# Optimization experiments

Measured on AMD Instinct MI355X. Metric: run time of the kernel, lower is better.

Reference implementation:

```python
import jax, jax.numpy as jnp
import numpy as np
from jax import lax

B, P, DIM, HEADS, K = 2, 4096, 256, 8, 32
DH = DIM // HEADS
SCALE = DH ** -0.5


def setup_inputs() -> dict:
    key = jax.random.key(0)
    ks = jax.random.split(key, 12)
    s = 0.02
    return {
        "xyz": jax.random.uniform(ks[0], (B, P, 3), dtype=jnp.float32),
        "feats": jax.random.normal(ks[1], (B, P, DIM), dtype=jnp.float32),
        "Wq": jax.random.normal(ks[2], (DIM, DIM), dtype=jnp.float32) * s,
        "Wk": jax.random.normal(ks[3], (DIM, DIM), dtype=jnp.float32) * s,
        "Wv": jax.random.normal(ks[4], (DIM, DIM), dtype=jnp.float32) * s,
        "Wp": jax.random.normal(ks[5], (DIM, DIM), dtype=jnp.float32) * s,
        "bp": jnp.zeros((DIM,), jnp.float32),
        "W1": jax.random.normal(ks[6], (DIM, 3), dtype=jnp.float32) * s,
        "b1": jnp.zeros((DIM,), jnp.float32),
        "W2": jax.random.normal(ks[7], (DIM, DIM), dtype=jnp.float32) * s,
        "b2": jnp.zeros((DIM,), jnp.float32),
    }


def _gather(points, idx):
    # points: (B,N,C), idx: (B,M,K) -> (B,M,K,C)
    return jax.vmap(lambda p, i: p[i])(points, idx)


def reference(xyz, feats, Wq, Wk, Wv, Wp, bp, W1, b1, W2, b2):
    b, p, d = feats.shape
    # kNN via squared euclidean distance (same ordering as cdist)
    d2 = jnp.sum((xyz[:, :, None, :] - xyz[:, None, :, :]) ** 2, axis=-1)  # (B,P,P)
    _, idx = lax.top_k(-d2, K)  # (B,P,K) smallest distances

    neigh_xyz = _gather(xyz, idx)                      # (B,P,K,3)
    relpos = neigh_xyz - xyz[:, :, None, :]            # (B,P,K,3)

    q = (feats @ Wq.T).reshape(b, p, HEADS, DH)        # (B,P,H,Dh)
    k_full = feats @ Wk.T                              # (B,P,D)
    v_full = feats @ Wv.T
    k_nei = _gather(k_full, idx).reshape(b, p, K, HEADS, DH)
    v_nei = _gather(v_full, idx).reshape(b, p, K, HEADS, DH)

    # pos MLP: Linear(3,dim) -> ReLU -> Linear(dim,dim)
    h = jax.nn.relu(relpos @ W1.T + b1)
    pos_bias = (h @ W2.T + b2).reshape(b, p, K, HEADS, DH)

    attn = jnp.einsum('bphd,bpkhd->bpkh', q, k_nei + pos_bias) * SCALE
    attn = jax.nn.softmax(attn, axis=2)                # over K neighbors
    out = jnp.einsum('bpkh,bpkhd->bphd', attn, v_nei + pos_bias).reshape(b, p, d)
    return out @ Wp.T + bp
```

## Files before the change

kernel.cpp:

```cpp
#include <hip/hip_runtime.h>
#include <cstddef>

#define PB 4096
static constexpr float SCALE_F = 0.17677669529663687f;

typedef __attribute__((ext_vector_type(8))) short bf16x8;
typedef __attribute__((ext_vector_type(4))) float f32x4;

static __device__ __forceinline__ unsigned short f2bf(float x) {
  unsigned u = __builtin_bit_cast(unsigned, x);
  u += 0x7fffu + ((u >> 16) & 1u);
  return (unsigned short)(u >> 16);
}
static __device__ __forceinline__ float bf2f(unsigned short h) {
  return __builtin_bit_cast(float, (unsigned)h << 16);
}

__global__ __launch_bounds__(256) void knn_kernel(const float* __restrict__ xyz,
                                                  int* __restrict__ idx_out) {
  __shared__ float xs[768];
  const int wid = threadIdx.x >> 6;
  const int lane = threadIdx.x & 63;
  const int g = (blockIdx.x << 2) + wid;
  const int b = g >> 12;
  const int p = g & (PB - 1);
  const float* base = xyz + (size_t)b * PB * 3;
  const float qx = base[p * 3 + 0];
  const float qy = base[p * 3 + 1];
  const float qz = base[p * 3 + 2];
  float list_d = 3.4e38f;
  int list_i = -1;
  for (int c = 0; c < 16; ++c) {
    __syncthreads();
    const int src = c * 768 + threadIdx.x;
    xs[threadIdx.x]       = base[src];
    xs[threadIdx.x + 256] = base[src + 256];
    xs[threadIdx.x + 512] = base[src + 512];
    __syncthreads();
#pragma unroll
    for (int s = 0; s < 4; ++s) {
      const int jl = (s << 6) + lane;
      const float dx = __fsub_rn(qx, xs[jl * 3 + 0]);
      const float dy = __fsub_rn(qy, xs[jl * 3 + 1]);
      const float dz = __fsub_rn(qz, xs[jl * 3 + 2]);
      const float d2 = __fadd_rn(__fadd_rn(__fmul_rn(dx, dx), __fmul_rn(dy, dy)),
                                 __fmul_rn(dz, dz));
      float worst = __shfl(list_d, 31);
      unsigned long long mask = __ballot(d2 < worst);
      while (mask) {
        const int l = __ffsll(mask) - 1;
        mask &= mask - 1;
        const float v = __shfl(d2, l);
        worst = __shfl(list_d, 31);
        if (v < worst) {
          const unsigned long long gt = __ballot((lane < 32) && (list_d > v));
          const int pos = __ffsll(gt) - 1;
          const float pd = __shfl_up(list_d, 1);
          const int pi = __shfl_up(list_i, 1);
          if (lane < 32 && lane >= pos) {
            const bool at = (lane == pos);
            list_d = at ? v : pd;
            list_i = at ? ((c << 8) + (s << 6) + l) : pi;
          }
        }
      }
    }
  }
  if (lane < 32) idx_out[(size_t)g * 32 + lane] = list_i;
}

__global__ __launch_bounds__(256) void prep_all(
    const float* __restrict__ Wq, const float* __restrict__ Wk,
    const float* __restrict__ Wv, const float* __restrict__ Wp,
    const float* __restrict__ W2, const float* __restrict__ b2,
    const float* __restrict__ bp,
    unsigned short* __restrict__ whi, unsigned short* __restrict__ wlo,
    unsigned short* __restrict__ w2bf, unsigned short* __restrict__ wqu_t,
    unsigned short* __restrict__ wop_t, float* __restrict__ bpp) {
  __shared__ float sbuf[32];
  const int blk = blockIdx.x;
  const int tid = threadIdx.x;
  if (blk < 1024) {
    const int e = blk * 256 + tid;
    const int m = e >> 16;
    const int off = e & 65535;
    const float* src = (m == 0) ? Wq : (m == 1) ? Wk : (m == 2) ? Wv : Wp;
    const float x = src[off];
    const unsigned short hi = f2bf(x);
    whi[e] = hi;
    wlo[e] = f2bf(x - bf2f(hi));
  } else if (blk < 1280) {
    const int off = (blk - 1024) * 256 + tid;
    w2bf[off] = f2bf(W2[off]);
  } else if (blk < 3328) {
    const int hm = blk - 1280;
    const int h = hm >> 8;
    const int m = hm & 255;
    if (tid < 32) sbuf[tid] = W2[(size_t)((h << 5) + tid) * 256 + m];
    __syncthreads();
    float a = 0.f;
#pragma unroll 8
    for (int t = 0; t < 32; ++t)
      a += Wq[(size_t)((h << 5) + t) * 256 + tid] * sbuf[t];
    wqu_t[(size_t)hm * 256 + tid] = f2bf(a);
  } else if (blk < 5376) {
    const int e = blk - 3328;
    const int j = e & 255;
    const int h = e >> 8;
    if (tid < 32) sbuf[tid] = Wp[(size_t)j * 256 + (h << 5) + tid];
    __syncthreads();
    float a = 0.f;
#pragma unroll 8
    for (int t = 0; t < 32; ++t)
      a += W2[(size_t)((h << 5) + t) * 256 + tid] * sbuf[t];
    wop_t[(size_t)j * 2048 + (h << 8) + tid] = f2bf(a);
  } else {
    const int j = blk - 5376;
    float v = b2[tid] * Wp[(size_t)j * 256 + tid];
#pragma unroll
    for (int off = 32; off; off >>= 1) v += __shfl_xor(v, off);
    if ((tid & 63) == 0) sbuf[tid >> 6] = v;
    __syncthreads();
    if (tid == 0) bpp[j] = bp[j] + sbuf[0] + sbuf[1] + sbuf[2] + sbuf[3];
  }
}

static __device__ __forceinline__ void gemm32_core(
    const float* __restrict__ A, const unsigned short* __restrict__ wh,
    const unsigned short* __restrict__ wl, const int r0,
    unsigned short* ah, unsigned short* al, f32x4 acc[2][4]) {
  const int tid = threadIdx.x;
#pragma unroll
  for (int t = 0; t < 8; ++t) {
    const int idx4 = (t << 8) + tid;
    const int row = idx4 >> 6;
    const int c4 = idx4 & 63;
    const float4 v = *(const float4*)(A + (size_t)(r0 + row) * 256 + (c4 << 2));
    const unsigned short h0 = f2bf(v.x), h1 = f2bf(v.y);
    const unsigned short h2 = f2bf(v.z), h3 = f2bf(v.w);
    const unsigned short l0 = f2bf(v.x - bf2f(h0)), l1 = f2bf(v.y - bf2f(h1));
    const unsigned short l2 = f2bf(v.z - bf2f(h2)), l3 = f2bf(v.w - bf2f(h3));
    const int base = (row << 9) + ((c4 << 3) ^ ((row & 7) << 4));
    *(uint2*)((char*)ah + base) =
        make_uint2((unsigned)h0 | ((unsigned)h1 << 16),
                   (unsigned)h2 | ((unsigned)h3 << 16));
    *(uint2*)((char*)al + base) =
        make_uint2((unsigned)l0 | ((unsigned)l1 << 16),
                   (unsigned)l2 | ((unsigned)l3 << 16));
  }
  __syncthreads();
  const int lane = tid & 63;
  const int w = tid >> 6;
  const int il = lane & 15;
  const int q4 = lane >> 4;
#pragma unroll
  for (int mt = 0; mt < 2; ++mt)
#pragma unroll
    for (int nt = 0; nt < 4; ++nt) acc[mt][nt] = (f32x4){0.f, 0.f, 0.f, 0.f};
#pragma unroll 2
  for (int ks = 0; ks < 8; ++ks) {
    bf16x8 bh[4], bl[4], a0[2], a1[2];
#pragma unroll
    for (int nt = 0; nt < 4; ++nt) {
      const int n = (w << 6) + (nt << 4) + il;
      const size_t off = (size_t)n * 256 + (ks << 5) + (q4 << 3);
      bh[nt] = *(const bf16x8*)(wh + off);
      bl[nt] = *(const bf16x8*)(wl + off);
    }
#pragma unroll
    for (int mt = 0; mt < 2; ++mt) {
      const int row = (mt << 4) + il;
      const int byte = (row << 9) + ((((ks << 5) + (q4 << 3)) << 1) ^ ((row & 7) << 4));
      a0[mt] = *(const bf16x8*)((const char*)ah + byte);
      a1[mt] = *(const bf16x8*)((const char*)al + byte);
    }
#pragma unroll
    for (int mt = 0; mt < 2; ++mt)
#pragma unroll
      for (int nt = 0; nt < 4; ++nt) {
        acc[mt][nt] = __builtin_amdgcn_mfma_f32_16x16x32_bf16(a0[mt], bh[nt], acc[mt][nt], 0, 0, 0);
        acc[mt][nt] = __builtin_amdgcn_mfma_f32_16x16x32_bf16(a1[mt], bh[nt], acc[mt][nt], 0, 0, 0);
        acc[mt][nt] = __builtin_amdgcn_mfma_f32_16x16x32_bf16(a0[mt], bl[nt], acc[mt][nt], 0, 0, 0);
      }
  }
}

__global__ __launch_bounds__(256) void qkvu_mfma(
    const float* __restrict__ feats,
    const unsigned short* __restrict__ whi, const unsigned short* __restrict__ wlo,
    const unsigned short* __restrict__ wqu_t,
    float* __restrict__ qb, unsigned short* __restrict__ kb16,
    unsigned short* __restrict__ vb16, unsigned short* __restrict__ U) {
  __shared__ __align__(16) unsigned short ah[32 * 256];
  __shared__ __align__(16) unsigned short al[32 * 256];
  const int bid = blockIdx.x;
  const int tid = threadIdx.x;
  const int lane = tid & 63;
  const int w = tid >> 6;
  const int il = lane & 15;
  const int q4 = lane >> 4;
  if (bid < 768) {
    const int sel = bid % 3;
    const int r0 = (bid / 3) << 5;
    const unsigned short* wh = whi + (size_t)sel * 65536;
    const unsigned short* wl = wlo + (size_t)sel * 65536;
    f32x4 acc[2][4];
    gemm32_core(feats, wh, wl, r0, ah, al, acc);
#pragma unroll
    for (int mt = 0; mt < 2; ++mt)
#pragma unroll
      for (int nt = 0; nt < 4; ++nt) {
        const int col = (w << 6) + (nt << 4) + il;
#pragma unroll
        for (int r = 0; r < 4; ++r) {
          const size_t e = (size_t)(r0 + (mt << 4) + (q4 << 2) + r) * 256 + col;
          if (sel == 0) qb[e] = acc[mt][nt][r];
          else if (sel == 1) kb16[e] = f2bf(acc[mt][nt][r]);
          else vb16[e] = f2bf(acc[mt][nt][r]);
        }
      }
  } else {
    const int t = bid - 768;
    const int r0 = (t & 255) << 5;
    const int cb = t >> 8;
#pragma unroll
    for (int tt = 0; tt < 8; ++tt) {
      const int idx4 = (tt << 8) + tid;
      const int row = idx4 >> 6;
      const int c4 = idx4 & 63;
      const float4 v = *(const float4*)(feats + (size_t)(r0 + row) * 256 + (c4 << 2));
      const int base = (row << 9) + ((c4 << 3) ^ ((row & 7) << 4));
      *(uint2*)((char*)ah + base) =
          make_uint2((unsigned)f2bf(v.x) | ((unsigned)f2bf(v.y) << 16),
                     (unsigned)f2bf(v.z) | ((unsigned)f2bf(v.w) << 16));
    }
    __syncthreads();
    const unsigned short* wh = wqu_t + (size_t)cb * 65536;
    f32x4 acc[2][4];
#pragma unroll
    for (int mt = 0; mt < 2; ++mt)
#pragma unroll
      for (int nt = 0; nt < 4; ++nt) acc[mt][nt] = (f32x4){0.f, 0.f, 0.f, 0.f};
#pragma unroll 2
    for (int ks = 0; ks < 8; ++ks) {
      bf16x8 bh[4], a0[2];
#pragma unroll
      for (int nt = 0; nt < 4; ++nt) {
        const int n = (w << 6) + (nt << 4) + il;
        bh[nt] = *(const bf16x8*)(wh + (size_t)n * 256 + (ks << 5) + (q4 << 3));
      }
#pragma unroll
      for (int mt = 0; mt < 2; ++mt) {
        const int row = (mt << 4) + il;
        const int byte = (row << 9) + ((((ks << 5) + (q4 << 3)) << 1) ^ ((row & 7) << 4));
        a0[mt] = *(const bf16x8*)((const char*)ah + byte);
      }
#pragma unroll
      for (int mt = 0; mt < 2; ++mt)
#pragma unroll
        for (int nt = 0; nt < 4; ++nt)
          acc[mt][nt] = __builtin_amdgcn_mfma_f32_16x16x32_bf16(a0[mt], bh[nt], acc[mt][nt], 0, 0, 0);
    }
#pragma unroll
    for (int mt = 0; mt < 2; ++mt)
#pragma unroll
      for (int nt = 0; nt < 4; ++nt) {
        const int col = (w << 6) + (nt << 4) + il;
#pragma unroll
        for (int r = 0; r < 4; ++r)
          U[(size_t)(r0 + (mt << 4) + (q4 << 2) + r) * 2048 + (cb << 8) + col] =
              f2bf(acc[mt][nt][r]);
      }
  }
}

template <bool FOLD>
__global__ __launch_bounds__(256) void proj_mfma(
    const float* __restrict__ A,
    const unsigned short* __restrict__ whi, const unsigned short* __restrict__ wlo,
    const unsigned short* __restrict__ c16, const unsigned short* __restrict__ wop_t,
    const float* __restrict__ bias, float* __restrict__ C) {
  __shared__ __align__(16) unsigned short ah[32 * 256];
  __shared__ __align__(16) unsigned short al[32 * 256];
  const int r0 = blockIdx.x << 5;
  f32x4 acc[2][4];
  gemm32_core(A, whi, wlo, r0, ah, al, acc);
  const int tid = threadIdx.x;
  const int lane = tid & 63;
  const int w = tid >> 6;
  const int il = lane & 15;
  const int q4 = lane >> 4;
  if (FOLD) {
#pragma unroll 4
    for (int ks2 = 0; ks2 < 64; ++ks2) {
      bf16x8 af[2];
#pragma unroll
      for (int mt = 0; mt < 2; ++mt)
        af[mt] = *(const bf16x8*)(c16 + (size_t)(r0 + (mt << 4) + il) * 2048 +
                                  (ks2 << 5) + (q4 << 3));
#pragma unroll
      for (int nt = 0; nt < 4; ++nt) {
        const int n = (w << 6) + (nt << 4) + il;
        const bf16x8 bf = *(const bf16x8*)(wop_t + (size_t)n * 2048 +
                                           (ks2 << 5) + (q4 << 3));
#pragma unroll
        for (int mt = 0; mt < 2; ++mt)
          acc[mt][nt] = __builtin_amdgcn_mfma_f32_16x16x32_bf16(af[mt], bf, acc[mt][nt], 0, 0, 0);
      }
    }
  }
#pragma unroll
  for (int mt = 0; mt < 2; ++mt)
#pragma unroll
    for (int nt = 0; nt < 4; ++nt) {
      const int col = (w << 6) + (nt << 4) + il;
      const float bv = bias[col];
#pragma unroll
      for (int r = 0; r < 4; ++r)
        C[(size_t)(r0 + (mt << 4) + (q4 << 2) + r) * 256 + col] = acc[mt][nt][r] + bv;
    }
}

__global__ __launch_bounds__(256) void fused_big(
    const float* __restrict__ xyz, const int* __restrict__ nbr_idx,
    const float* __restrict__ qbuf, const unsigned short* __restrict__ kb16,
    const unsigned short* __restrict__ vb16,
    const float* __restrict__ W1, const float* __restrict__ b1,
    const unsigned short* __restrict__ ubuf,
    unsigned short* __restrict__ c16, float* __restrict__ o_pre) {
  __shared__ __align__(16) unsigned short h_km[32 * 256];
  __shared__ __align__(16) char h_mk[256 * 80];
  __shared__ __align__(16) unsigned short u16l[16 * 256];
  __shared__ float sc_part[4][32][9];
  __shared__ __align__(16) char at16[16 * 80];
  __shared__ float q_lds[256];
  __shared__ float rel[32][3];
  __shared__ int nbr_s[32];

  const int g = blockIdx.x;
  const int b = g >> 12;
  const int p = g & (PB - 1);
  const int tid = threadIdx.x;

  if (tid < 32) {
    const int j = nbr_idx[(size_t)g * 32 + tid];
    nbr_s[tid] = j;
    const float* xb = xyz + (size_t)b * PB * 3;
    rel[tid][0] = xb[j * 3 + 0] - xb[p * 3 + 0];
    rel[tid][1] = xb[j * 3 + 1] - xb[p * 3 + 1];
    rel[tid][2] = xb[j * 3 + 2] - xb[p * 3 + 2];
  }
  q_lds[tid] = qbuf[(size_t)g * 256 + tid];
  *(uint4*)((char*)u16l + 4096 + tid * 16) = make_uint4(0, 0, 0, 0);
  if (tid < 160) *(unsigned*)(at16 + 640 + tid * 4) = 0;
  __syncthreads();

  {
    const int half = tid >> 7;
    const int c0 = (tid & 127) << 1;
    const int stg = (tid >> 1) & 7;
    const float w00 = W1[c0 * 3 + 0], w01 = W1[c0 * 3 + 1], w02 = W1[c0 * 3 + 2];
    const float w10 = W1[c0 * 3 + 3], w11 = W1[c0 * 3 + 4], w12 = W1[c0 * 3 + 5];
    const float bb0 = b1[c0], bb1 = b1[c0 + 1];
#pragma unroll 4
    for (int rl = 0; rl < 16; ++rl) {
      const int rr = (half << 4) | ((rl + stg) & 15);
      const float rx = rel[rr][0], ry = rel[rr][1], rz = rel[rr][2];
      const float h0 = fmaxf(bb0 + rx * w00 + ry * w01 + rz * w02, 0.f);
      const float h1 = fmaxf(bb1 + rx * w10 + ry * w11 + rz * w12, 0.f);
      const unsigned short bh0 = f2bf(h0), bh1 = f2bf(h1);
      *(unsigned*)((char*)h_km + (rr << 9) + (((unsigned)c0 << 1) ^ ((rr & 7) << 4))) =
          (unsigned)bh0 | ((unsigned)bh1 << 16);
      *(unsigned short*)(h_mk + c0 * 80 + rr * 2) = bh0;
      *(unsigned short*)(h_mk + (c0 + 1) * 80 + rr * 2) = bh1;
    }
  }
  {
    const int h = tid >> 5;
    const int byte = (h << 9) + ((((tid & 31) << 4)) ^ ((h & 7) << 4));
    const uint4 uv = *(const uint4*)(ubuf + (size_t)g * 2048 + tid * 8);
    *(uint4*)((char*)u16l + byte) = uv;
  }
  __syncthreads();

  const int lane = tid & 63;
  const int w = tid >> 6;
  const int il = lane & 15;
  const int q4 = lane >> 4;
  const int kk = tid & 31;
  const int hh = tid >> 5;

  float sqk = 0.f;
  {
    const int j = nbr_s[kk];
    const unsigned short* krow = kb16 + ((size_t)(b << 12) + j) * 256 + (hh << 5);
#pragma unroll
    for (int c4 = 0; c4 < 4; ++c4) {
      const bf16x8 kv = *(const bf16x8*)(krow + (c4 << 3));
#pragma unroll
      for (int jj = 0; jj < 8; ++jj)
        sqk += q_lds[(hh << 5) + (c4 << 3) + jj] * bf2f((unsigned short)kv[jj]);
    }
  }
  {
    f32x4 accp[2];
    accp[0] = (f32x4){0.f, 0.f, 0.f, 0.f};
    accp[1] = (f32x4){0.f, 0.f, 0.f, 0.f};
#pragma unroll
    for (int ksl = 0; ksl < 2; ++ksl) {
      const int m0 = (w << 6) + (ksl << 5) + (q4 << 3);
      const bf16x8 bfr = *(const bf16x8*)((char*)u16l + (il << 9) +
                                          (((unsigned)m0 << 1) ^ ((il & 7) << 4)));
#pragma unroll
      for (int mt = 0; mt < 2; ++mt) {
        const int row = (mt << 4) + il;
        const bf16x8 afr = *(const bf16x8*)((char*)h_km + (row << 9) +
                                            (((unsigned)m0 << 1) ^ ((row & 7) << 4)));
        accp[mt] = __builtin_amdgcn_mfma_f32_16x16x32_bf16(afr, bfr, accp[mt], 0, 0, 0);
      }
    }
    if (il < 8) {
#pragma unroll
      for (int mt = 0; mt < 2; ++mt)
#pragma unroll
        for (int r = 0; r < 4; ++r)
          sc_part[w][(mt << 4) + (q4 << 2) + r][il] = accp[mt][r];
    }
  }
  __syncthreads();

  {
    float s = sqk + sc_part[0][kk][hh] + sc_part[1][kk][hh] +
              sc_part[2][kk][hh] + sc_part[3][kk][hh];
    s *= SCALE_F;
    float mx = s;
#pragma unroll
    for (int off = 16; off; off >>= 1) mx = fmaxf(mx, __shfl_xor(mx, off));
    const float e = __expf(s - mx);
    float ssum = e;
#pragma unroll
    for (int off = 16; off; off >>= 1) ssum += __shfl_xor(ssum, off);
    *(unsigned short*)(at16 + hh * 80 + kk * 2) = f2bf(e / ssum);
  }
  __syncthreads();

  {
    const bf16x8 afr = *(const bf16x8*)(at16 + il * 80 + (q4 << 4));
    const f32x4 zero = (f32x4){0.f, 0.f, 0.f, 0.f};
#pragma unroll
    for (int nt = 0; nt < 4; ++nt) {
      const int m = (w << 6) + (nt << 4) + il;
      const bf16x8 bfr = *(const bf16x8*)(h_mk + m * 80 + (q4 << 4));
      const f32x4 c = __builtin_amdgcn_mfma_f32_16x16x32_bf16(afr, bfr, zero, 0, 0, 0);
      if (q4 < 2) {
#pragma unroll
        for (int r = 0; r < 4; ++r)
          c16[(size_t)g * 2048 + (size_t)((q4 << 2) + r) * 256 + m] = f2bf(c[r]);
      }
    }
  }

  {
    const int n = tid;
    const int h = n >> 5;
    float o = 0.f;
    const size_t vbase = (size_t)(b << 12) * 256 + n;
#pragma unroll 4
    for (int k = 0; k < 32; ++k) {
      const float aw = bf2f(*(const unsigned short*)(at16 + h * 80 + k * 2));
      o += aw * bf2f(vb16[vbase + (size_t)nbr_s[k] * 256]);
    }
    o_pre[(size_t)g * 256 + n] = o;
  }
}

__global__ __launch_bounds__(256) void fused_small(
    const float* __restrict__ xyz, const int* __restrict__ nbr_idx,
    const float* __restrict__ qbuf, const unsigned short* __restrict__ kb16,
    const unsigned short* __restrict__ vb16,
    const float* __restrict__ W1, const float* __restrict__ b1,
    const unsigned short* __restrict__ w2bf, const float* __restrict__ b2,
    float* __restrict__ o_pre) {
  __shared__ __align__(16) unsigned short h_lds[32 * 256];
  __shared__ float q_lds[256];
  __shared__ float u_lds[8][256];
  __shared__ float c_lds[8][256];
  __shared__ float at_lds[32][8];
  __shared__ float rel[32][3];
  __shared__ int nbr_s[32];

  const int g = blockIdx.x;
  const int b = g >> 12;
  const int p = g & (PB - 1);
  const int tid = threadIdx.x;

  if (tid < 32) {
    const int j = nbr_idx[(size_t)g * 32 + tid];
    nbr_s[tid] = j;
    const float* xb = xyz + (size_t)b * PB * 3;
    rel[tid][0] = xb[j * 3 + 0] - xb[p * 3 + 0];
    rel[tid][1] = xb[j * 3 + 1] - xb[p * 3 + 1];
    rel[tid][2] = xb[j * 3 + 2] - xb[p * 3 + 2];
  }
  q_lds[tid] = qbuf[(size_t)g * 256 + tid];
  __syncthreads();

  {
    const int half = tid >> 7;
    const int c0 = (tid & 127) << 1;
    const float w00 = W1[c0 * 3 + 0], w01 = W1[c0 * 3 + 1], w02 = W1[c0 * 3 + 2];
    const float w10 = W1[c0 * 3 + 3], w11 = W1[c0 * 3 + 4], w12 = W1[c0 * 3 + 5];
    const float bb0 = b1[c0], bb1 = b1[c0 + 1];
#pragma unroll 4
    for (int rl = 0; rl < 16; ++rl) {
      const int rr = (half << 4) + rl;
      const float rx = rel[rr][0], ry = rel[rr][1], rz = rel[rr][2];
      const float h0 = fmaxf(bb0 + rx * w00 + ry * w01 + rz * w02, 0.f);
      const float h1 = fmaxf(bb1 + rx * w10 + ry * w11 + rz * w12, 0.f);
      const unsigned pk = (unsigned)f2bf(h0) | ((unsigned)f2bf(h1) << 16);
      *(unsigned*)((char*)h_lds + (rr << 9) + (((unsigned)c0 << 1) ^ ((rr & 7) << 4))) = pk;
    }
  }
  {
    const int h = tid >> 5;
    const int m8 = (tid & 31) << 3;
    float ua[8];
#pragma unroll
    for (int j = 0; j < 8; ++j) ua[j] = 0.f;
    const unsigned short* wrow = w2bf + (size_t)(h << 5) * 256 + m8;
#pragma unroll 4
    for (int i = 0; i < 32; ++i) {
      const float qn = q_lds[(h << 5) + i];
      const bf16x8 wv = *(const bf16x8*)(wrow + (size_t)i * 256);
#pragma unroll
      for (int j = 0; j < 8; ++j) ua[j] += qn * bf2f((unsigned short)wv[j]);
    }
#pragma unroll
    for (int j = 0; j < 8; ++j) u_lds[h][m8 + j] = ua[j];
  }
  __syncthreads();

  {
    const int k = tid & 31;
    const int h = tid >> 5;
    const int j = nbr_s[k];
    const unsigned short* krow = kb16 + ((size_t)(b << 12) + j) * 256 + (h << 5);
    float s = 0.f;
#pragma unroll
    for (int c4 = 0; c4 < 4; ++c4) {
      const bf16x8 kv = *(const bf16x8*)(krow + (c4 << 3));
#pragma unroll
      for (int jj = 0; jj < 8; ++jj)
        s += q_lds[(h << 5) + (c4 << 3) + jj] * bf2f((unsigned short)kv[jj]);
    }
#pragma unroll 4
    for (int m8 = 0; m8 < 32; ++m8) {
      const bf16x8 hv = *(const bf16x8*)((const char*)h_lds + (k << 9) +
                                         ((m8 << 4) ^ ((k & 7) << 4)));
      const float4 u0 = *(const float4*)&u_lds[h][m8 << 3];
      const float4 u1 = *(const float4*)&u_lds[h][(m8 << 3) + 4];
      s += u0.x * bf2f((unsigned short)hv[0]) + u0.y * bf2f((unsigned short)hv[1]) +
           u0.z * bf2f((unsigned short)hv[2]) + u0.w * bf2f((unsigned short)hv[3]) +
           u1.x * bf2f((unsigned short)hv[4]) + u1.y * bf2f((unsigned short)hv[5]) +
           u1.z * bf2f((unsigned short)hv[6]) + u1.w * bf2f((unsigned short)hv[7]);
    }
    s *= SCALE_F;
    float mx = s;
#pragma unroll
    for (int off = 16; off; off >>= 1) mx = fmaxf(mx, __shfl_xor(mx, off));
    const float e = __expf(s - mx);
    float ssum = e;
#pragma unroll
    for (int off = 16; off; off >>= 1) ssum += __shfl_xor(ssum, off);
    at_lds[k][h] = e / ssum;
  }
  __syncthreads();

  {
    const int m = tid;
    float ca[8];
#pragma unroll
    for (int h = 0; h < 8; ++h) ca[h] = 0.f;
#pragma unroll 4
    for (int k = 0; k < 32; ++k) {
      const float hv = bf2f(*(const unsigned short*)(
          (const char*)h_lds + (k << 9) + ((2 * m) ^ ((k & 7) << 4))));
      const float4 a0 = *(const float4*)&at_lds[k][0];
      const float4 a1 = *(const float4*)&at_lds[k][4];
      ca[0] += a0.x * hv; ca[1] += a0.y * hv; ca[2] += a0.z * hv; ca[3] += a0.w * hv;
      ca[4] += a1.x * hv; ca[5] += a1.y * hv; ca[6] += a1.z * hv; ca[7] += a1.w * hv;
    }
#pragma unroll
    for (int h = 0; h < 8; ++h) c_lds[h][m] = ca[h];
  }
  __syncthreads();

  {
    const int n = tid;
    const int h = n >> 5;
    float o = b2[n];
    const size_t vbase = (size_t)(b << 12) * 256 + n;
#pragma unroll 4
    for (int k = 0; k < 32; ++k)
      o += at_lds[k][h] * bf2f(vb16[vbase + (size_t)nbr_s[k] * 256]);
    const unsigned short* wrow = w2bf + (size_t)n * 256;
    float opos = 0.f;
#pragma unroll 4
    for (int m8 = 0; m8 < 32; ++m8) {
      const bf16x8 wv = *(const bf16x8*)(wrow + (m8 << 3));
      const float4 c0 = *(const float4*)&c_lds[h][m8 << 3];
      const float4 c1 = *(const float4*)&c_lds[h][(m8 << 3) + 4];
      opos += c0.x * bf2f((unsigned short)wv[0]) + c0.y * bf2f((unsigned short)wv[1]) +
              c0.z * bf2f((unsigned short)wv[2]) + c0.w * bf2f((unsigned short)wv[3]) +
              c1.x * bf2f((unsigned short)wv[4]) + c1.y * bf2f((unsigned short)wv[5]) +
              c1.z * bf2f((unsigned short)wv[6]) + c1.w * bf2f((unsigned short)wv[7]);
    }
    o_pre[(size_t)g * 256 + n] = o + opos;
  }
}

extern "C" void kernel_launch(void* const* d_in, const int* in_sizes, int n_in,
                              void* d_out, int out_size, void* d_ws, size_t ws_size,
                              hipStream_t stream) {
  (void)in_sizes; (void)n_in; (void)out_size;
  const float* xyz   = (const float*)d_in[0];
  const float* feats = (const float*)d_in[1];
  const float* Wq    = (const float*)d_in[2];
  const float* Wk    = (const float*)d_in[3];
  const float* Wv    = (const float*)d_in[4];
  const float* Wp    = (const float*)d_in[5];
  const float* bp    = (const float*)d_in[6];
  const float* W1    = (const float*)d_in[7];
  const float* b1    = (const float*)d_in[8];
  const float* W2    = (const float*)d_in[9];
  const float* b2    = (const float*)d_in[10];
  float* out = (float*)d_out;

  float* wsf = (float*)d_ws;
  int* idxw            = (int*)wsf;
  float* qb            = wsf + 262144;
  unsigned short* kb16 = (unsigned short*)(wsf + 2359296);
  unsigned short* vb16 = (unsigned short*)(wsf + 3407872);
  float* op            = wsf + 4456448;
  unsigned short* whi  = (unsigned short*)(wsf + 6553600);
  unsigned short* wlo  = (unsigned short*)(wsf + 6684672);
  unsigned short* w2bf = (unsigned short*)(wsf + 6815744);
  unsigned short* wqut = (unsigned short*)(wsf + 6848512);
  unsigned short* wopt = (unsigned short*)(wsf + 7110656);
  float* bpp           = wsf + 7372800;
  unsigned short* c16  = (unsigned short*)(wsf + 7373056);
  const bool big = ws_size >= (size_t)15761664 * 4;

  hipLaunchKernelGGL(prep_all, dim3(big ? 5632 : 1280), dim3(256), 0, stream,
                     Wq, Wk, Wv, Wp, W2, b2, bp, whi, wlo, w2bf, wqut, wopt, bpp);
  hipLaunchKernelGGL(knn_kernel, dim3(2 * PB / 4), dim3(256), 0, stream, xyz, idxw);
  hipLaunchKernelGGL(qkvu_mfma, dim3(big ? 2816 : 768), dim3(256), 0, stream,
                     feats, whi, wlo, wqut, qb, kb16, vb16, c16);
  if (big) {
    hipLaunchKernelGGL(fused_big, dim3(2 * PB), dim3(256), 0, stream,
                       xyz, idxw, qb, kb16, vb16, W1, b1, c16, c16, op);
    hipLaunchKernelGGL(proj_mfma<true>, dim3(256), dim3(256), 0, stream,
                       op, whi + (size_t)3 * 65536, wlo + (size_t)3 * 65536,
                       c16, wopt, bpp, out);
  } else {
    hipLaunchKernelGGL(fused_small, dim3(2 * PB), dim3(256), 0, stream,
                       xyz, idxw, qb, kb16, vb16, W1, b1, w2bf, b2, op);
    hipLaunchKernelGGL(proj_mfma<false>, dim3(256), dim3(256), 0, stream,
                       op, whi + (size_t)3 * 65536, wlo + (size_t)3 * 65536,
                       nullptr, nullptr, bp, out);
  }
}
```

Baseline: 346.1 us.

## Stage GEMM outputs through LDS for coalesced stores and tile U GEMM larger

Output tiles of the q/k/v and U GEMMs are now written to shared memory first and then stored to global memory as wide vector stores, replacing scattered 2- and 4-byte writes. The U-projection blocks now cover 64 rows instead of 32, which cuts the grid and reuses each weight fragment across more rows. The folded projection stages c16 tiles in swizzled LDS before the MFMA loop, and fused_big packs its c16 output through LDS so it can be written coalesced. The cost is extra barriers, more LDS per block and more accumulator registers in the U path.

```diff
diff --git a/kernel.cpp b/kernel.cpp
--- a/kernel.cpp
+++ b/kernel.cpp
@@ -191,8 +191,9 @@
     const unsigned short* __restrict__ wqu_t,
     float* __restrict__ qb, unsigned short* __restrict__ kb16,
     unsigned short* __restrict__ vb16, unsigned short* __restrict__ U) {
-  __shared__ __align__(16) unsigned short ah[32 * 256];
-  __shared__ __align__(16) unsigned short al[32 * 256];
+  __shared__ __align__(16) unsigned short smem[64 * 256];
+  unsigned short* ah = smem;
+  unsigned short* al = smem + 32 * 256;
   const int bid = blockIdx.x;
   const int tid = threadIdx.x;
   const int lane = tid & 63;
@@ -202,75 +203,101 @@
   if (bid < 768) {
     const int sel = bid % 3;
     const int r0 = (bid / 3) << 5;
-    const unsigned short* wh = whi + (size_t)sel * 65536;
-    const unsigned short* wl = wlo + (size_t)sel * 65536;
     f32x4 acc[2][4];
-    gemm32_core(feats, wh, wl, r0, ah, al, acc);
-#pragma unroll
-    for (int mt = 0; mt < 2; ++mt)
-#pragma unroll
-      for (int nt = 0; nt < 4; ++nt) {
-        const int col = (w << 6) + (nt << 4) + il;
-#pragma unroll
-        for (int r = 0; r < 4; ++r) {
-          const size_t e = (size_t)(r0 + (mt << 4) + (q4 << 2) + r) * 256 + col;
-          if (sel == 0) qb[e] = acc[mt][nt][r];
-          else if (sel == 1) kb16[e] = f2bf(acc[mt][nt][r]);
-          else vb16[e] = f2bf(acc[mt][nt][r]);
-        }
-      }
+    gemm32_core(feats, whi + (size_t)sel * 65536, wlo + (size_t)sel * 65536,
+                r0, ah, al, acc);
+    __syncthreads();
+    if (sel == 0) {
+      float* fb = (float*)smem;
+#pragma unroll
+      for (int mt = 0; mt < 2; ++mt)
+#pragma unroll
+        for (int nt = 0; nt < 4; ++nt)
+#pragma unroll
+          for (int r = 0; r < 4; ++r)
+            fb[((mt << 4) + (q4 << 2) + r) * 256 + (w << 6) + (nt << 4) + il] =
+                acc[mt][nt][r];
+      __syncthreads();
+      float* dst = qb + (size_t)r0 * 256;
+#pragma unroll
+      for (int i = 0; i < 8; ++i)
+        *(float4*)(dst + tid * 32 + (i << 2)) = *(float4*)(fb + tid * 32 + (i << 2));
+    } else {
+#pragma unroll
+      for (int mt = 0; mt < 2; ++mt)
+#pragma unroll
+        for (int nt = 0; nt < 4; ++nt)
+#pragma unroll
+          for (int r = 0; r < 4; ++r)
+            smem[((mt << 4) + (q4 << 2) + r) * 256 + (w << 6) + (nt << 4) + il] =
+                f2bf(acc[mt][nt][r]);
+      __syncthreads();
+      unsigned short* dst = ((sel == 1) ? kb16 : vb16) + (size_t)r0 * 256;
+#pragma unroll
+      for (int i = 0; i < 4; ++i)
+        *(uint4*)(dst + tid * 32 + (i << 3)) = *(uint4*)(smem + tid * 32 + (i << 3));
+    }
   } else {
     const int t = bid - 768;
-    const int r0 = (t & 255) << 5;
-    const int cb = t >> 8;
-#pragma unroll
-    for (int tt = 0; tt < 8; ++tt) {
+    const int r0 = (t & 127) << 6;
+    const int cb = t >> 7;
+#pragma unroll
+    for (int tt = 0; tt < 16; ++tt) {
       const int idx4 = (tt << 8) + tid;
       const int row = idx4 >> 6;
       const int c4 = idx4 & 63;
       const float4 v = *(const float4*)(feats + (size_t)(r0 + row) * 256 + (c4 << 2));
       const int base = (row << 9) + ((c4 << 3) ^ ((row & 7) << 4));
-      *(uint2*)((char*)ah + base) =
+      *(uint2*)((char*)smem + base) =
           make_uint2((unsigned)f2bf(v.x) | ((unsigned)f2bf(v.y) << 16),
                      (unsigned)f2bf(v.z) | ((unsigned)f2bf(v.w) << 16));
     }
     __syncthreads();
     const unsigned short* wh = wqu_t + (size_t)cb * 65536;
-    f32x4 acc[2][4];
-#pragma unroll
-    for (int mt = 0; mt < 2; ++mt)
+    f32x4 acc[4][4];
+#pragma unroll
+    for (int mt = 0; mt < 4; ++mt)
 #pragma unroll
       for (int nt = 0; nt < 4; ++nt) acc[mt][nt] = (f32x4){0.f, 0.f, 0.f, 0.f};
 #pragma unroll 2
     for (int ks = 0; ks < 8; ++ks) {
-      bf16x8 bh[4], a0[2];
+      bf16x8 bh[4], a0[4];
 #pragma unroll
       for (int nt = 0; nt < 4; ++nt) {
         const int n = (w << 6) + (nt << 4) + il;
         bh[nt] = *(const bf16x8*)(wh + (size_t)n * 256 + (ks << 5) + (q4 << 3));
       }
 #pragma unroll
-      for (int mt = 0; mt < 2; ++mt) {
+      for (int mt = 0; mt < 4; ++mt) {
         const int row = (mt << 4) + il;
         const int byte = (row << 9) + ((((ks << 5) + (q4 << 3)) << 1) ^ ((row & 7) << 4));
-        a0[mt] = *(const bf16x8*)((const char*)ah + byte);
+        a0[mt] = *(const bf16x8*)((const char*)smem + byte);
       }
 #pragma unroll
-      for (int mt = 0; mt < 2; ++mt)
+      for (int mt = 0; mt < 4; ++mt)
 #pragma unroll
         for (int nt = 0; nt < 4; ++nt)
           acc[mt][nt] = __builtin_amdgcn_mfma_f32_16x16x32_bf16(a0[mt], bh[nt], acc[mt][nt], 0, 0, 0);
     }
-#pragma unroll
-    for (int mt = 0; mt < 2; ++mt)
-#pragma unroll
-      for (int nt = 0; nt < 4; ++nt) {
-        const int col = (w << 6) + (nt << 4) + il;
+    __syncthreads();
+#pragma unroll
+    for (int mt = 0; mt < 4; ++mt)
+#pragma unroll
+      for (int nt = 0; nt < 4; ++nt)
 #pragma unroll
         for (int r = 0; r < 4; ++r)
-          U[(size_t)(r0 + (mt << 4) + (q4 << 2) + r) * 2048 + (cb << 8) + col] =
+          smem[((mt << 4) + (q4 << 2) + r) * 256 + (w << 6) + (nt << 4) + il] =
               f2bf(acc[mt][nt][r]);
-      }
+    __syncthreads();
+    {
+      const int row = tid >> 2;
+      const int c0 = (tid & 3) << 6;
+      unsigned short* dst = U + (size_t)(r0 + row) * 2048 + (cb << 8) + c0;
+      const unsigned short* srcl = smem + row * 256 + c0;
+#pragma unroll
+      for (int i = 0; i < 8; ++i)
+        *(uint4*)(dst + (i << 3)) = *(const uint4*)(srcl + (i << 3));
+    }
   }
 }
 
@@ -280,8 +307,9 @@
     const unsigned short* __restrict__ whi, const unsigned short* __restrict__ wlo,
     const unsigned short* __restrict__ c16, const unsigned short* __restrict__ wop_t,
     const float* __restrict__ bias, float* __restrict__ C) {
-  __shared__ __align__(16) unsigned short ah[32 * 256];
-  __shared__ __align__(16) unsigned short al[32 * 256];
+  __shared__ __align__(16) unsigned short smem[64 * 256];
+  unsigned short* ah = smem;
+  unsigned short* al = smem + 32 * 256;
   const int r0 = blockIdx.x << 5;
   f32x4 acc[2][4];
   gemm32_core(A, whi, wlo, r0, ah, al, acc);
@@ -291,21 +319,36 @@
   const int il = lane & 15;
   const int q4 = lane >> 4;
   if (FOLD) {
-#pragma unroll 4
-    for (int ks2 = 0; ks2 < 64; ++ks2) {
-      bf16x8 af[2];
-#pragma unroll
-      for (int mt = 0; mt < 2; ++mt)
-        af[mt] = *(const bf16x8*)(c16 + (size_t)(r0 + (mt << 4) + il) * 2048 +
-                                  (ks2 << 5) + (q4 << 3));
-#pragma unroll
-      for (int nt = 0; nt < 4; ++nt) {
-        const int n = (w << 6) + (nt << 4) + il;
-        const bf16x8 bf = *(const bf16x8*)(wop_t + (size_t)n * 2048 +
-                                           (ks2 << 5) + (q4 << 3));
-#pragma unroll
-        for (int mt = 0; mt < 2; ++mt)
-          acc[mt][nt] = __builtin_amdgcn_mfma_f32_16x16x32_bf16(af[mt], bf, acc[mt][nt], 0, 0, 0);
+    for (int ch = 0; ch < 16; ++ch) {
+      __syncthreads();
+#pragma unroll
+      for (int pass = 0; pass < 2; ++pass) {
+        const int idx = (pass << 8) + tid;
+        const int row = idx >> 4;
+        const int c16i = idx & 15;
+        const uint4 v = *(const uint4*)(c16 + (size_t)(r0 + row) * 2048 +
+                                        (ch << 7) + (c16i << 3));
+        *(uint4*)((char*)smem + row * 256 + ((c16i << 4) ^ ((row & 7) << 4))) = v;
+      }
+      __syncthreads();
+#pragma unroll
+      for (int sub = 0; sub < 4; ++sub) {
+        bf16x8 af[2];
+#pragma unroll
+        for (int mt = 0; mt < 2; ++mt) {
+          const int row = (mt << 4) + il;
+          af[mt] = *(const bf16x8*)((const char*)smem + row * 256 +
+                                    (((sub << 6) + (q4 << 4)) ^ ((row & 7) << 4)));
+        }
+#pragma unroll
+        for (int nt = 0; nt < 4; ++nt) {
+          const int n = (w << 6) + (nt << 4) + il;
+          const bf16x8 bf = *(const bf16x8*)(wop_t + (size_t)n * 2048 +
+                                             (ch << 7) + (sub << 5) + (q4 << 3));
+#pragma unroll
+          for (int mt = 0; mt < 2; ++mt)
+            acc[mt][nt] = __builtin_amdgcn_mfma_f32_16x16x32_bf16(af[mt], bf, acc[mt][nt], 0, 0, 0);
+        }
       }
     }
   }
@@ -331,11 +374,12 @@
   __shared__ __align__(16) unsigned short h_km[32 * 256];
   __shared__ __align__(16) char h_mk[256 * 80];
   __shared__ __align__(16) unsigned short u16l[16 * 256];
-  __shared__ float sc_part[4][32][9];
+  __shared__ __align__(16) char scpad[4608];
   __shared__ __align__(16) char at16[16 * 80];
   __shared__ float q_lds[256];
   __shared__ float rel[32][3];
   __shared__ int nbr_s[32];
+  float (*sc_part)[32][9] = (float (*)[32][9])scpad;
 
   const int g = blockIdx.x;
   const int b = g >> 12;
@@ -445,6 +489,7 @@
   __syncthreads();
 
   {
+    unsigned short* c8b = (unsigned short*)scpad;
     const bf16x8 afr = *(const bf16x8*)(at16 + il * 80 + (q4 << 4));
     const f32x4 zero = (f32x4){0.f, 0.f, 0.f, 0.f};
 #pragma unroll
@@ -455,9 +500,11 @@
       if (q4 < 2) {
 #pragma unroll
         for (int r = 0; r < 4; ++r)
-          c16[(size_t)g * 2048 + (size_t)((q4 << 2) + r) * 256 + m] = f2bf(c[r]);
+          c8b[((q4 << 2) + r) * 256 + m] = f2bf(c[r]);
       }
     }
+    __syncthreads();
+    *(uint4*)(c16 + (size_t)g * 2048 + tid * 8) = *(const uint4*)(c8b + tid * 8);
   }
 
   {
@@ -654,7 +701,7 @@
   hipLaunchKernelGGL(prep_all, dim3(big ? 5632 : 1280), dim3(256), 0, stream,
                      Wq, Wk, Wv, Wp, W2, b2, bp, whi, wlo, w2bf, wqut, wopt, bpp);
   hipLaunchKernelGGL(knn_kernel, dim3(2 * PB / 4), dim3(256), 0, stream, xyz, idxw);
-  hipLaunchKernelGGL(qkvu_mfma, dim3(big ? 2816 : 768), dim3(256), 0, stream,
+  hipLaunchKernelGGL(qkvu_mfma, dim3(big ? 1792 : 768), dim3(256), 0, stream,
                      feats, whi, wlo, wqut, qb, kb16, vb16, c16);
   if (big) {
     hipLaunchKernelGGL(fused_big, dim3(2 * PB), dim3(256), 0, stream,
```

New measurement: 340.8 us. Within noise of the previous version (-1.5%).
